# Optimization experiments

Hardware: AMD Instinct MI355X
Metric: run time of the kernel (lower is better)

## Reference

```python
import jax, jax.numpy as jnp
import numpy as np


def setup_inputs() -> dict:
    key = jax.random.key(0)
    k1, k2, k3, k4, k5 = jax.random.split(key, 5)
    N, IN, OUT = 4096, 2048, 2048
    return {
        "input": jax.random.normal(k1, (N, IN), dtype=jnp.float32),
        "weight_mu": jax.random.normal(k2, (OUT, IN), dtype=jnp.float32) * 0.25,
        "weight_rho": jax.random.normal(k3, (OUT, IN), dtype=jnp.float32) - 5.0,
        "eps_weight": jax.random.normal(k4, (OUT, IN), dtype=jnp.float32),
        "bias": jax.random.normal(k5, (OUT,), dtype=jnp.float32) * 0.02,
    }


def reference(input, weight_mu, weight_rho, eps_weight, bias):
    # Effective weight: mu + softplus(rho) * eps   (log1p(exp(rho)) == softplus)
    w = weight_mu + jax.nn.softplus(weight_rho) * eps_weight  # [out, in]
    # F.linear: input @ w.T + bias
    return jnp.einsum("ni,oi->no", input, w) + bias
```

## Files before the change

### kernel.cpp

```cpp
#include <hip/hip_runtime.h>
#include <stdint.h>

typedef __bf16 bf16x8 __attribute__((ext_vector_type(8)));
typedef float f32x4 __attribute__((ext_vector_type(4)));
typedef float float4v __attribute__((ext_vector_type(4)));
typedef unsigned short u16x8 __attribute__((ext_vector_type(8)));

__device__ __forceinline__ unsigned short f2bf(float f) {
    unsigned u = __float_as_uint(f);
    u += 0x7fffu + ((u >> 16) & 1u);
    return (unsigned short)(u >> 16);
}

__device__ __forceinline__ float softplus(float x) {
    return fmaxf(x, 0.0f) + __logf(1.0f + __expf(-fabsf(x)));
}

__device__ __forceinline__ void gl_lds16(const void* gptr, void* lptr) {
    auto g = reinterpret_cast<const __attribute__((address_space(1))) void*>(
        reinterpret_cast<uintptr_t>(gptr));
    auto l = reinterpret_cast<__attribute__((address_space(3))) void*>(
        reinterpret_cast<uintptr_t>(lptr));
    __builtin_amdgcn_global_load_lds(g, l, 16, 0, 0);
}

__global__ void prep_kernel(const float* __restrict__ in,
                            const float* __restrict__ mu,
                            const float* __restrict__ rho,
                            const float* __restrict__ eps,
                            unsigned short* __restrict__ in_bf,
                            unsigned short* __restrict__ w_bf,
                            int nIn8, int nW8) {
    int i = blockIdx.x * blockDim.x + threadIdx.x;
    if (i < nIn8) {
        const float4v* p = (const float4v*)in + (size_t)i * 2;
        float4v a = p[0], b = p[1];
        u16x8 r;
        r[0] = f2bf(a[0]); r[1] = f2bf(a[1]); r[2] = f2bf(a[2]); r[3] = f2bf(a[3]);
        r[4] = f2bf(b[0]); r[5] = f2bf(b[1]); r[6] = f2bf(b[2]); r[7] = f2bf(b[3]);
        ((u16x8*)in_bf)[i] = r;
    } else {
        int j = i - nIn8;
        if (j >= nW8) return;
        const float4v* pm = (const float4v*)mu  + (size_t)j * 2;
        const float4v* pr = (const float4v*)rho + (size_t)j * 2;
        const float4v* pe = (const float4v*)eps + (size_t)j * 2;
        float4v m0 = pm[0], m1 = pm[1];
        float4v r0 = pr[0], r1 = pr[1];
        float4v e0 = pe[0], e1 = pe[1];
        u16x8 r;
        r[0] = f2bf(m0[0] + softplus(r0[0]) * e0[0]);
        r[1] = f2bf(m0[1] + softplus(r0[1]) * e0[1]);
        r[2] = f2bf(m0[2] + softplus(r0[2]) * e0[2]);
        r[3] = f2bf(m0[3] + softplus(r0[3]) * e0[3]);
        r[4] = f2bf(m1[0] + softplus(r1[0]) * e1[0]);
        r[5] = f2bf(m1[1] + softplus(r1[1]) * e1[1]);
        r[6] = f2bf(m1[2] + softplus(r1[2]) * e1[2]);
        r[7] = f2bf(m1[3] + softplus(r1[3]) * e1[3]);
        ((u16x8*)w_bf)[j] = r;
    }
}

#define BM 128
#define BN 128
#define BK 64

__global__ __launch_bounds__(512, 4)
void gemm_bt_kernel(const unsigned short* __restrict__ A,
                    const unsigned short* __restrict__ B,
                    const float* __restrict__ bias,
                    float* __restrict__ C,
                    int M, int N, int K) {
    __shared__ unsigned short lds_a[BM * BK];
    __shared__ unsigned short lds_b[BN * BK];

    const int t      = threadIdx.x;
    const int lane   = t & 63;
    const int wave   = t >> 6;
    const int lane16 = lane & 15;
    const int quad   = lane >> 4;
    const int wm     = wave & 1;
    const int wn     = wave >> 1;

    const int m0 = blockIdx.y * BM;
    const int n0 = blockIdx.x * BN;

    const int r1   = t >> 3;
    const int pkg1 = t & 7;
    const int g1   = (pkg1 ^ (r1 & 7)) * 8;
    const int r2   = r1 + 64;
    const int g2   = (pkg1 ^ (r2 & 7)) * 8;

    const unsigned short* Ab = A + (size_t)m0 * K;
    const unsigned short* Bb = B + (size_t)n0 * K;

    f32x4 acc[4][2] = {};

    const int sw = lane16 & 7;

    for (int k0 = 0; k0 < K; k0 += BK) {
        gl_lds16(Ab + (size_t)r1 * K + k0 + g1, lds_a + t * 8);
        gl_lds16(Ab + (size_t)r2 * K + k0 + g2, lds_a + 4096 + t * 8);
        gl_lds16(Bb + (size_t)r1 * K + k0 + g1, lds_b + t * 8);
        gl_lds16(Bb + (size_t)r2 * K + k0 + g2, lds_b + 4096 + t * 8);
        __syncthreads();

#pragma unroll
        for (int ch = 0; ch < 2; ch++) {
            const int kg = ch * 4 + quad;
            const int pk = (kg ^ sw) * 8;
            bf16x8 af[4], bfr[2];
#pragma unroll
            for (int mi = 0; mi < 4; mi++)
                af[mi] = *(const bf16x8*)(lds_a + (wm * 64 + mi * 16 + lane16) * BK + pk);
#pragma unroll
            for (int ni = 0; ni < 2; ni++)
                bfr[ni] = *(const bf16x8*)(lds_b + (wn * 32 + ni * 16 + lane16) * BK + pk);
#pragma unroll
            for (int mi = 0; mi < 4; mi++)
#pragma unroll
                for (int ni = 0; ni < 2; ni++)
                    acc[mi][ni] = __builtin_amdgcn_mfma_f32_16x16x32_bf16(
                        af[mi], bfr[ni], acc[mi][ni], 0, 0, 0);
        }
        __syncthreads();
    }

    float bv[2];
#pragma unroll
    for (int ni = 0; ni < 2; ni++)
        bv[ni] = bias[n0 + wn * 32 + ni * 16 + lane16];

#pragma unroll
    for (int mi = 0; mi < 4; mi++) {
        const int rbase = m0 + wm * 64 + mi * 16 + quad * 4;
#pragma unroll
        for (int ni = 0; ni < 2; ni++) {
            const int col = n0 + wn * 32 + ni * 16 + lane16;
#pragma unroll
            for (int r = 0; r < 4; r++)
                C[(size_t)(rbase + r) * N + col] = acc[mi][ni][r] + bv[ni];
        }
    }
}

extern "C" void kernel_launch(void* const* d_in, const int* in_sizes, int n_in,
                              void* d_out, int out_size, void* d_ws, size_t ws_size,
                              hipStream_t stream) {
    const float* input = (const float*)d_in[0];
    const float* mu    = (const float*)d_in[1];
    const float* rho   = (const float*)d_in[2];
    const float* eps   = (const float*)d_in[3];
    const float* bias  = (const float*)d_in[4];
    float* out = (float*)d_out;

    const int OUT = in_sizes[4];
    const int IN  = in_sizes[1] / OUT;
    const int M   = in_sizes[0] / IN;

    unsigned short* in_bf = (unsigned short*)d_ws;
    unsigned short* w_bf  = in_bf + (size_t)M * IN;

    const int nIn8 = (M * IN) / 8;
    const int nW8  = (OUT * IN) / 8;
    prep_kernel<<<dim3((nIn8 + nW8 + 255) / 256), 256, 0, stream>>>(
        input, mu, rho, eps, in_bf, w_bf, nIn8, nW8);

    gemm_bt_kernel<<<dim3(OUT / BN, M / BM), 512, 0, stream>>>(
        in_bf, w_bf, bias, out, M, OUT, IN);
}
```

Before: 161.4 us.

## Double-buffer LDS tiles to overlap global loads with MFMA compute

```diff
diff --git a/kernel.cpp b/kernel.cpp
--- a/kernel.cpp
+++ b/kernel.cpp
@@ -71,8 +71,8 @@
                     const float* __restrict__ bias,
                     float* __restrict__ C,
                     int M, int N, int K) {
-    __shared__ unsigned short lds_a[BM * BK];
-    __shared__ unsigned short lds_b[BN * BK];
+    __shared__ unsigned short lds_a[2][BM * BK];
+    __shared__ unsigned short lds_b[2][BN * BK];
 
     const int t      = threadIdx.x;
     const int lane   = t & 63;
@@ -95,35 +95,48 @@
     const unsigned short* Bb = B + (size_t)n0 * K;
 
     f32x4 acc[4][2] = {};
-
     const int sw = lane16 & 7;
 
-    for (int k0 = 0; k0 < K; k0 += BK) {
-        gl_lds16(Ab + (size_t)r1 * K + k0 + g1, lds_a + t * 8);
-        gl_lds16(Ab + (size_t)r2 * K + k0 + g2, lds_a + 4096 + t * 8);
-        gl_lds16(Bb + (size_t)r1 * K + k0 + g1, lds_b + t * 8);
-        gl_lds16(Bb + (size_t)r2 * K + k0 + g2, lds_b + 4096 + t * 8);
-        __syncthreads();
+    auto stage = [&](int buf, int k0) {
+        gl_lds16(Ab + (size_t)r1 * K + k0 + g1, &lds_a[buf][t * 8]);
+        gl_lds16(Ab + (size_t)r2 * K + k0 + g2, &lds_a[buf][4096 + t * 8]);
+        gl_lds16(Bb + (size_t)r1 * K + k0 + g1, &lds_b[buf][t * 8]);
+        gl_lds16(Bb + (size_t)r2 * K + k0 + g2, &lds_b[buf][4096 + t * 8]);
+    };
 
+    const int nit = K / BK;
+    stage(0, 0);
+    __syncthreads();
+
+    auto body = [&](int cur, int it) {
+        const unsigned short* la = lds_a[cur];
+        const unsigned short* lb = lds_b[cur];
+        bf16x8 af[2][4], bfr[2][2];
 #pragma unroll
         for (int ch = 0; ch < 2; ch++) {
-            const int kg = ch * 4 + quad;
-            const int pk = (kg ^ sw) * 8;
-            bf16x8 af[4], bfr[2];
+            const int pk = ((ch * 4 + quad) ^ sw) * 8;
 #pragma unroll
             for (int mi = 0; mi < 4; mi++)
-                af[mi] = *(const bf16x8*)(lds_a + (wm * 64 + mi * 16 + lane16) * BK + pk);
+                af[ch][mi] = *(const bf16x8*)(la + (wm * 64 + mi * 16 + lane16) * BK + pk);
 #pragma unroll
             for (int ni = 0; ni < 2; ni++)
-                bfr[ni] = *(const bf16x8*)(lds_b + (wn * 32 + ni * 16 + lane16) * BK + pk);
+                bfr[ch][ni] = *(const bf16x8*)(lb + (wn * 32 + ni * 16 + lane16) * BK + pk);
+        }
+        if (it + 1 < nit) stage(cur ^ 1, (it + 1) * BK);
+#pragma unroll
+        for (int ch = 0; ch < 2; ch++)
 #pragma unroll
             for (int mi = 0; mi < 4; mi++)
 #pragma unroll
                 for (int ni = 0; ni < 2; ni++)
                     acc[mi][ni] = __builtin_amdgcn_mfma_f32_16x16x32_bf16(
-                        af[mi], bfr[ni], acc[mi][ni], 0, 0, 0);
-        }
+                        af[ch][mi], bfr[ch][ni], acc[mi][ni], 0, 0, 0);
         __syncthreads();
+    };
+
+    for (int it = 0; it < nit; it += 2) {
+        body(0, it);
+        body(1, it + 1);
     }
 
     float bv[2];
```

New measurement: 159.9 us. No clear change (-0.9%).
